# Performance work log

Hardware: AMD Instinct MI355X
Metric: run time of the kernel (lower is better)

## Reference

```python
import jax, jax.numpy as jnp
from jax import lax
import numpy as np

B, T, F, U, O = 512, 512, 128, 256, 32  # batch, max_t, joint feature dim, lstm units, n_output


def setup_inputs() -> dict:
    key = jax.random.key(0)
    k = jax.random.split(key, 6)
    return {
        "x_joint": jax.random.normal(k[0], (B, T, F), dtype=jnp.float32),
        "Wx": jax.random.normal(k[1], (F, 4 * U), dtype=jnp.float32) / np.sqrt(F).astype(np.float32),
        "Wh": jax.random.normal(k[2], (U, 4 * U), dtype=jnp.float32) / np.sqrt(U).astype(np.float32),
        "b": jnp.zeros((4 * U,), dtype=jnp.float32),
        "Wo": jax.random.normal(k[3], (U, O), dtype=jnp.float32) / np.sqrt(U).astype(np.float32),
        "bo": jnp.zeros((O,), dtype=jnp.float32),
        "seq_lengths": jax.random.randint(k[4], (B,), 0, T, dtype=jnp.int32),
    }


def reference(x_joint, Wx, Wh, b, Wo, bo, seq_lengths):
    """Masked LSTM decoder scan with per-step Dense projection.

    Flax nn.RNN(DecoderLSTMCell): LSTMCell gates i,f,g,o then Dense(n_output).
    With return_carry=True + seq_lengths, flax only uses seq_lengths to slice the
    final carry, which RNNSurrogate discards; outputs are the full per-step
    predictions, so seq_lengths does not enter the returned math.
    """
    bsz, t, _ = x_joint.shape
    units = Wh.shape[0]
    # precompute input contribution to all 4 gates: [B, T, 4U]
    x_proj = jnp.einsum('btf,fg->btg', x_joint, Wx) + b
    c0 = jnp.zeros((bsz, units), dtype=x_joint.dtype)
    h0 = jnp.zeros((bsz, units), dtype=x_joint.dtype)

    def step(carry, xt):
        c, h = carry
        z = xt + h @ Wh  # [B, 4U]
        i, f, g, o = jnp.split(z, 4, axis=-1)
        c = jax.nn.sigmoid(f) * c + jax.nn.sigmoid(i) * jnp.tanh(g)
        h = jax.nn.sigmoid(o) * jnp.tanh(c)
        y = h @ Wo + bo  # per-step Dense projection
        return (c, h), y

    _, ys = lax.scan(step, (c0, h0), x_proj.transpose(1, 0, 2))  # ys: [T, B, O]
    return ys.transpose(1, 0, 2)  # [B, T, O]
```

## Files before the change

### kernel.cpp

```cpp
#include <hip/hip_runtime.h>
#include <stdint.h>

#define BB 512
#define TT 512
#define FF 128
#define UU 256

typedef float f32x4 __attribute__((ext_vector_type(4)));
typedef short short8 __attribute__((ext_vector_type(8)));
typedef int int4v __attribute__((ext_vector_type(4)));
typedef float float4v __attribute__((ext_vector_type(4)));
typedef unsigned short ushort4v __attribute__((ext_vector_type(4)));

__device__ __forceinline__ unsigned short f2bf(float f) {
  union { float f; uint32_t u; } v; v.f = f;
  uint32_t u = v.u;
  u += 0x7fffu + ((u >> 16) & 1u);
  return (unsigned short)(u >> 16);
}
__device__ __forceinline__ float fast_rcp(float x) { return __builtin_amdgcn_rcpf(x); }
__device__ __forceinline__ float sigmoidf_(float x) { return fast_rcp(1.f + __expf(-x)); }
__device__ __forceinline__ float tanhf_(float x) { return 1.f - 2.f * fast_rcp(1.f + __expf(2.f * x)); }

__global__ void prep_w(const float* __restrict__ Wx, const float* __restrict__ Wh,
                       const float* __restrict__ Wo,
                       unsigned short* __restrict__ Wt, unsigned short* __restrict__ Wot,
                       int* __restrict__ xch) {
  int bidx = blockIdx.x;
  int tid = threadIdx.x;
  if (bidx < 1024) {
    int n = bidx, k = tid;
    float v = (k < FF) ? Wx[(size_t)k * 1024 + n] : Wh[(size_t)(k - FF) * 1024 + n];
    Wt[(size_t)n * 384 + k] = f2bf(v);
  } else if (bidx == 1024) {
    for (int i = tid; i < 32 * 256; i += 384) {
      int o = i >> 8, u = i & 255;
      Wot[o * 256 + u] = f2bf(Wo[(size_t)u * 32 + o]);
    }
  } else {
    int base = (bidx - 1025) * 2048;
    for (int i = tid; i < 2048; i += 384) xch[base + i] = 0;
  }
}

__global__ void conv_x(const float* __restrict__ xf, unsigned short* __restrict__ xb) {
  size_t i = (size_t)blockIdx.x * 1024 + (size_t)threadIdx.x * 4;
  float4v v = *(const float4v*)(xf + i);
  ushort4v o;
  o.x = f2bf(v.x); o.y = f2bf(v.y); o.z = f2bf(v.z); o.w = f2bf(v.w);
  *(ushort4v*)(xb + i) = o;
}

__device__ __forceinline__ short8 load_xfrag(const unsigned short* p) {
  return *(const short8*)p;
}
__device__ __forceinline__ short8 load_xfrag(const float* p) {
  float4v lo = *(const float4v*)p;
  float4v hi = *(const float4v*)(p + 4);
  union { short8 v; unsigned short s[8]; } a;
  a.s[0] = f2bf(lo.x); a.s[1] = f2bf(lo.y); a.s[2] = f2bf(lo.z); a.s[3] = f2bf(lo.w);
  a.s[4] = f2bf(hi.x); a.s[5] = f2bf(hi.y); a.s[6] = f2bf(hi.z); a.s[7] = f2bf(hi.w);
  return a.v;
}

__device__ __forceinline__ void store_sc01(int* p, int v) {
  asm volatile("global_store_dword %0, %1, off sc0 sc1" :: "v"(p), "v"(v) : "memory");
}
__device__ __forceinline__ uint32_t pk2(int lo, int hi) {
  return ((uint32_t)lo >> 16) | ((uint32_t)hi & 0xffff0000u);
}

template <int HALF, typename XT>
__device__ __forceinline__ void lstm_core(const XT* __restrict__ x,
                                          const unsigned short* __restrict__ Wt,
                                          const float* __restrict__ bvec,
                                          unsigned short* __restrict__ h_hist,
                                          int* __restrict__ xch, int bid, char* lds) {
  const int mt = bid & 31;
  const int tid = threadIdx.x;
  const int w = tid >> 6, l = tid & 63;
  const int lr = l & 15, lhi = l >> 4;
  const int b0 = mt * 16;
  const int uloc = HALF * 128 + w * 16 + lr;
  char* hlds = lds + 131072;
  char* plds = lds + 139264;

#pragma unroll
  for (int g = 0; g < 4; ++g)
#pragma unroll
    for (int kk = 0; kk < 4; ++kk) {
      const unsigned short* wp = Wt + (size_t)(g * 256 + uloc) * 384 + kk * 32 + 8 * lhi;
      *(short8*)(lds + ((size_t)((w * 16 + g * 4 + kk) * 64 + l)) * 16) = *(const short8*)wp;
    }

  short8 Bh[4][8];
#pragma unroll
  for (int g = 0; g < 4; ++g) {
    const unsigned short* wp = Wt + (size_t)(g * 256 + uloc) * 384 + FF + 8 * lhi;
#pragma unroll
    for (int kf = 0; kf < 8; ++kf) Bh[g][kf] = *(const short8*)(wp + kf * 32);
  }
  float bias[4];
#pragma unroll
  for (int g = 0; g < 4; ++g) bias[g] = bvec[g * 256 + uloc];
  float cst[4] = {0.f, 0.f, 0.f, 0.f};

  constexpr int kf_own = HALF * 4;
  constexpr int kf_par = (1 - HALF) * 4;

  const int rtile = (mt * 2 + (1 - HALF)) * 2;
  const int wtile = (mt * 2 + HALF) * 2;

  const int prow = tid >> 5;
  const int pwbyte = (prow * 256 + (tid & 31) * 8) ^ ((prow & 7) << 4);

  short8 xa[4];
  {
    const XT* xp = x + ((size_t)(b0 + lr) * TT + 0) * FF + 8 * lhi;
#pragma unroll
    for (int kk = 0; kk < 4; ++kk) xa[kk] = load_xfrag(xp + kk * 32);
  }
  __syncthreads();

#pragma unroll 1
  for (int t = 0; t < TT; ++t) {
    const int cur = t & 1, nxt = cur ^ 1;

    f32x4 acc[4];
#pragma unroll
    for (int g = 0; g < 4; ++g) { f32x4 a4 = {bias[g], bias[g], bias[g], bias[g]}; acc[g] = a4; }

    if (t > 0) {
      short8 ho[4];
#pragma unroll
      for (int ko = 0; ko < 4; ++ko) {
        const int byte = cur * 4096 + lr * 256 + ((ko * 64 + lhi * 16) ^ ((lr & 7) << 4));
        ho[ko] = *(const short8*)(hlds + byte);
      }
#pragma unroll
      for (int ko = 0; ko < 4; ++ko)
#pragma unroll
        for (int g = 0; g < 4; ++g)
          acc[g] = __builtin_amdgcn_mfma_f32_16x16x32_bf16(ho[ko], Bh[g][kf_own + ko], acc[g], 0, 0, 0);
    }

#pragma unroll
    for (int kk = 0; kk < 4; ++kk) {
      short8 bx[4];
#pragma unroll
      for (int g = 0; g < 4; ++g)
        bx[g] = *(const short8*)(lds + ((size_t)((w * 16 + g * 4 + kk) * 64 + l)) * 16);
#pragma unroll
      for (int g = 0; g < 4; ++g)
        acc[g] = __builtin_amdgcn_mfma_f32_16x16x32_bf16(xa[kk], bx[g], acc[g], 0, 0, 0);
    }

    {
      const int tn = (t + 1 < TT) ? t + 1 : t;
      const XT* xp = x + ((size_t)(b0 + lr) * TT + tn) * FF + 8 * lhi;
#pragma unroll
      for (int kk = 0; kk < 4; ++kk) xa[kk] = load_xfrag(xp + kk * 32);
    }

    if (t > 0) {
      const int* pp = xch + (rtile + cur) * 2048 + 4 * tid;
      int4v a;
      for (;;) {
        asm volatile("global_load_dwordx4 %0, %1, off sc0 sc1\n\ts_waitcnt vmcnt(0)"
                     : "=&v"(a) : "v"(pp) : "memory");
        int m = ((a.x ^ t) | (a.y ^ t) | (a.z ^ t) | (a.w ^ t)) & 0xffff;
        if (__all(m == 0)) break;
      }
      __builtin_amdgcn_sched_barrier(0);

      uint32_t d0 = pk2(a.x, a.y), d1 = pk2(a.z, a.w);
      *(uint64_t*)(plds + pwbyte) = ((uint64_t)d1 << 32) | d0;
      __syncthreads();

      short8 hq[4];
#pragma unroll
      for (int ko = 0; ko < 4; ++ko) {
        const int byte = (lr * 256 + lhi * 16 + ko * 64) ^ ((lr & 7) << 4);
        hq[ko] = *(const short8*)(plds + byte);
      }
#pragma unroll
      for (int ko = 0; ko < 4; ++ko)
#pragma unroll
        for (int g = 0; g < 4; ++g)
          acc[g] = __builtin_amdgcn_mfma_f32_16x16x32_bf16(hq[ko], Bh[g][kf_par + ko], acc[g], 0, 0, 0);
    }

    unsigned short hs[4];
#pragma unroll
    for (int r = 0; r < 4; ++r) {
      float zi = acc[0][r], zf = acc[1][r], zg = acc[2][r], zo = acc[3][r];
      float si = sigmoidf_(zi), sf = sigmoidf_(zf), so = sigmoidf_(zo);
      float tg = tanhf_(zg);
      float cn = sf * cst[r] + si * tg;
      cst[r] = cn;
      hs[r] = f2bf(so * tanhf_(cn));
    }

    const int wb = (wtile + nxt) * 2048 + w * 16 + lr;
    unsigned short* hw = h_hist + (size_t)(t + 1) * (BB * UU) + uloc;
#pragma unroll
    for (int r = 0; r < 4; ++r) {
      const int row = 4 * lhi + r;
      const int byte = nxt * 4096 + row * 256 + (((w * 16 + lr) * 2) ^ ((row & 7) << 4));
      *(unsigned short*)(hlds + byte) = hs[r];
      store_sc01(xch + wb + row * 128, ((int)(uint32_t)hs[r] << 16) | (t + 1));
      hw[(size_t)(b0 + row) * UU] = hs[r];
    }

    __syncthreads();
  }
}

template <typename XT>
__global__ void __launch_bounds__(512, 2)
lstm_main10(const XT* __restrict__ x, const unsigned short* __restrict__ Wt,
            const float* __restrict__ bvec, unsigned short* __restrict__ h_hist,
            int* __restrict__ xch) {
  __shared__ __align__(16) char lds[143360];
  const int bid = blockIdx.x;
  if (bid < 32) lstm_core<0, XT>(x, Wt, bvec, h_hist, xch, bid, lds);
  else          lstm_core<1, XT>(x, Wt, bvec, h_hist, xch, bid, lds);
}

__global__ void __launch_bounds__(256)
y_gemm(const unsigned short* __restrict__ h_hist, const unsigned short* __restrict__ Wot,
       const float* __restrict__ bo, float* __restrict__ out) {
  int gw = (int)((blockIdx.x * 256 + threadIdx.x) >> 6);
  int l = threadIdx.x & 63;
  int lr = l & 15, lhi = l >> 4;
  int b = gw >> 5;
  int t0 = (gw & 31) * 16;

  short8 Wf[2][8];
#pragma unroll
  for (int n = 0; n < 2; ++n) {
    const unsigned short* wp = Wot + (n * 16 + lr) * 256 + 8 * lhi;
#pragma unroll
    for (int kk = 0; kk < 8; ++kk) Wf[n][kk] = *(const short8*)(wp + kk * 32);
  }
  f32x4 acc[2];
#pragma unroll
  for (int n = 0; n < 2; ++n) {
    float bb = bo[n * 16 + lr];
    f32x4 a4 = {bb, bb, bb, bb};
    acc[n] = a4;
  }
  const unsigned short* hp =
      h_hist + ((size_t)(t0 + lr + 1) * BB + b) * UU + 8 * lhi;
#pragma unroll
  for (int kk = 0; kk < 8; ++kk) {
    short8 a = *(const short8*)(hp + kk * 32);
#pragma unroll
    for (int n = 0; n < 2; ++n)
      acc[n] = __builtin_amdgcn_mfma_f32_16x16x32_bf16(a, Wf[n][kk], acc[n], 0, 0, 0);
  }
#pragma unroll
  for (int n = 0; n < 2; ++n) {
    int o = n * 16 + lr;
#pragma unroll
    for (int r = 0; r < 4; ++r) {
      int t = t0 + 4 * lhi + r;
      out[((size_t)b * TT + t) * 32 + o] = acc[n][r];
    }
  }
}

extern "C" void kernel_launch(void* const* d_in, const int* in_sizes, int n_in,
                              void* d_out, int out_size, void* d_ws, size_t ws_size,
                              hipStream_t stream) {
  const float* x  = (const float*)d_in[0];
  const float* Wx = (const float*)d_in[1];
  const float* Wh = (const float*)d_in[2];
  const float* bv = (const float*)d_in[3];
  const float* Wo = (const float*)d_in[4];
  const float* bo = (const float*)d_in[5];

  char* ws = (char*)d_ws;
  size_t off = 0;
  int* xch = (int*)(ws + off);                          off += (size_t)262144 * 4;
  unsigned short* h_hist = (unsigned short*)(ws + off); off += (size_t)513 * BB * UU * 2;
  unsigned short* Wt384  = (unsigned short*)(ws + off); off += (size_t)1024 * 384 * 2;
  unsigned short* Wot    = (unsigned short*)(ws + off); off += (size_t)32 * 256 * 2;
  off = (off + 255) & ~(size_t)255;
  unsigned short* xb = (unsigned short*)(ws + off);
  const size_t need_xb = off + (size_t)BB * TT * FF * 2;

  prep_w<<<1153, 384, 0, stream>>>(Wx, Wh, Wo, Wt384, Wot, xch);
  if (ws_size >= need_xb) {
    conv_x<<<32768, 256, 0, stream>>>(x, xb);
    lstm_main10<unsigned short><<<64, 512, 0, stream>>>(xb, Wt384, bv, h_hist, xch);
  } else {
    lstm_main10<float><<<64, 512, 0, stream>>>(x, Wt384, bv, h_hist, xch);
  }
  y_gemm<<<4096, 256, 0, stream>>>(h_hist, Wot, bo, (float*)d_out);
}
```

Measured before the change: 1.483 ms.

## Fuse output projection into LSTM recurrence and drop h history buffer

Computes the per-step Dense projection inside the recurrent kernel: wave 0 of each block reuses the previous step's h fragments, already in registers, with Wo staged in LDS, and writes outputs lagged by two steps, with an epilogue for the last two timesteps. This removes the large global h_hist write (513×B×U bf16) and the separate y_gemm launch. It also issues the exchange load early, before the MFMA work, to overlap its latency, and reorders the xch stores ahead of the LDS writes. The cost is extra MFMA and LDS work on wave 0 on the serial critical path, plus more LDS per block.

```diff
diff --git a/kernel.cpp b/kernel.cpp
--- a/kernel.cpp
+++ b/kernel.cpp
@@ -73,8 +73,10 @@
 template <int HALF, typename XT>
 __device__ __forceinline__ void lstm_core(const XT* __restrict__ x,
                                           const unsigned short* __restrict__ Wt,
+                                          const unsigned short* __restrict__ Wot,
                                           const float* __restrict__ bvec,
-                                          unsigned short* __restrict__ h_hist,
+                                          const float* __restrict__ bo,
+                                          float* __restrict__ out,
                                           int* __restrict__ xch, int bid, char* lds) {
   const int mt = bid & 31;
   const int tid = threadIdx.x;
@@ -84,6 +86,7 @@
   const int uloc = HALF * 128 + w * 16 + lr;
   char* hlds = lds + 131072;
   char* plds = lds + 139264;
+  char* wolds = lds + 143360;
 
 #pragma unroll
   for (int g = 0; g < 4; ++g)
@@ -92,6 +95,13 @@
       const unsigned short* wp = Wt + (size_t)(g * 256 + uloc) * 384 + kk * 32 + 8 * lhi;
       *(short8*)(lds + ((size_t)((w * 16 + g * 4 + kk) * 64 + l)) * 16) = *(const short8*)wp;
     }
+  if (w == 0) {
+#pragma unroll
+    for (int kf = 0; kf < 8; ++kf) {
+      const unsigned short* src = Wot + (size_t)(HALF * 16 + lr) * 256 + kf * 32 + 8 * lhi;
+      *(short8*)(wolds + (size_t)(kf * 64 + l) * 16) = *(const short8*)src;
+    }
+  }
 
   short8 Bh[4][8];
 #pragma unroll
@@ -103,6 +113,7 @@
   float bias[4];
 #pragma unroll
   for (int g = 0; g < 4; ++g) bias[g] = bvec[g * 256 + uloc];
+  const float bob = bo[HALF * 16 + lr];
   float cst[4] = {0.f, 0.f, 0.f, 0.f};
 
   constexpr int kf_own = HALF * 4;
@@ -113,6 +124,8 @@
 
   const int prow = tid >> 5;
   const int pwbyte = (prow * 256 + (tid & 31) * 8) ^ ((prow & 7) << 4);
+
+  short8 ho[4], hq[4];
 
   short8 xa[4];
   {
@@ -125,13 +138,36 @@
 #pragma unroll 1
   for (int t = 0; t < TT; ++t) {
     const int cur = t & 1, nxt = cur ^ 1;
+    const int* pp = xch + (rtile + cur) * 2048 + 4 * tid;
+
+    int4v a;
+    if (t > 0) {
+      asm volatile("global_load_dwordx4 %0, %1, off sc0 sc1"
+                   : "=&v"(a) : "v"(pp) : "memory");
+    }
+
+    if (t >= 2 && w == 0) {
+      f32x4 yacc = {bob, bob, bob, bob};
+#pragma unroll
+      for (int ko = 0; ko < 4; ++ko) {
+        short8 wf = *(const short8*)(wolds + (size_t)((kf_own + ko) * 64 + l) * 16);
+        yacc = __builtin_amdgcn_mfma_f32_16x16x32_bf16(ho[ko], wf, yacc, 0, 0, 0);
+      }
+#pragma unroll
+      for (int ko = 0; ko < 4; ++ko) {
+        short8 wf = *(const short8*)(wolds + (size_t)((kf_par + ko) * 64 + l) * 16);
+        yacc = __builtin_amdgcn_mfma_f32_16x16x32_bf16(hq[ko], wf, yacc, 0, 0, 0);
+      }
+#pragma unroll
+      for (int r = 0; r < 4; ++r)
+        out[((size_t)(b0 + 4 * lhi + r) * TT + (t - 2)) * 32 + HALF * 16 + lr] = yacc[r];
+    }
 
     f32x4 acc[4];
 #pragma unroll
     for (int g = 0; g < 4; ++g) { f32x4 a4 = {bias[g], bias[g], bias[g], bias[g]}; acc[g] = a4; }
 
     if (t > 0) {
-      short8 ho[4];
 #pragma unroll
       for (int ko = 0; ko < 4; ++ko) {
         const int byte = cur * 4096 + lr * 256 + ((ko * 64 + lhi * 16) ^ ((lr & 7) << 4));
@@ -163,21 +199,17 @@
     }
 
     if (t > 0) {
-      const int* pp = xch + (rtile + cur) * 2048 + 4 * tid;
-      int4v a;
-      for (;;) {
+      asm volatile("s_waitcnt vmcnt(0)" ::: "memory");
+      __builtin_amdgcn_sched_barrier(0);
+      while (!__all(((((a.x ^ t) | (a.y ^ t)) | ((a.z ^ t) | (a.w ^ t))) & 0xffff) == 0)) {
         asm volatile("global_load_dwordx4 %0, %1, off sc0 sc1\n\ts_waitcnt vmcnt(0)"
                      : "=&v"(a) : "v"(pp) : "memory");
-        int m = ((a.x ^ t) | (a.y ^ t) | (a.z ^ t) | (a.w ^ t)) & 0xffff;
-        if (__all(m == 0)) break;
       }
       __builtin_amdgcn_sched_barrier(0);
 
       uint32_t d0 = pk2(a.x, a.y), d1 = pk2(a.z, a.w);
       *(uint64_t*)(plds + pwbyte) = ((uint64_t)d1 << 32) | d0;
       __syncthreads();
-
-      short8 hq[4];
 #pragma unroll
       for (int ko = 0; ko < 4; ++ko) {
         const int byte = (lr * 256 + lhi * 16 + ko * 64) ^ ((lr & 7) << 4);
@@ -202,72 +234,78 @@
     }
 
     const int wb = (wtile + nxt) * 2048 + w * 16 + lr;
-    unsigned short* hw = h_hist + (size_t)(t + 1) * (BB * UU) + uloc;
+#pragma unroll
+    for (int r = 0; r < 4; ++r)
+      store_sc01(xch + wb + (4 * lhi + r) * 128, ((int)(uint32_t)hs[r] << 16) | (t + 1));
 #pragma unroll
     for (int r = 0; r < 4; ++r) {
       const int row = 4 * lhi + r;
       const int byte = nxt * 4096 + row * 256 + (((w * 16 + lr) * 2) ^ ((row & 7) << 4));
       *(unsigned short*)(hlds + byte) = hs[r];
-      store_sc01(xch + wb + row * 128, ((int)(uint32_t)hs[r] << 16) | (t + 1));
-      hw[(size_t)(b0 + row) * UU] = hs[r];
     }
 
     __syncthreads();
+  }
+
+  if (w == 0) {
+    f32x4 yacc = {bob, bob, bob, bob};
+#pragma unroll
+    for (int ko = 0; ko < 4; ++ko) {
+      short8 wf = *(const short8*)(wolds + (size_t)((kf_own + ko) * 64 + l) * 16);
+      yacc = __builtin_amdgcn_mfma_f32_16x16x32_bf16(ho[ko], wf, yacc, 0, 0, 0);
+    }
+#pragma unroll
+    for (int ko = 0; ko < 4; ++ko) {
+      short8 wf = *(const short8*)(wolds + (size_t)((kf_par + ko) * 64 + l) * 16);
+      yacc = __builtin_amdgcn_mfma_f32_16x16x32_bf16(hq[ko], wf, yacc, 0, 0, 0);
+    }
+#pragma unroll
+    for (int r = 0; r < 4; ++r)
+      out[((size_t)(b0 + 4 * lhi + r) * TT + (TT - 2)) * 32 + HALF * 16 + lr] = yacc[r];
+  }
+  {
+    const int* pp = xch + (rtile + 0) * 2048 + 4 * tid;
+    int4v a;
+    do {
+      asm volatile("global_load_dwordx4 %0, %1, off sc0 sc1\n\ts_waitcnt vmcnt(0)"
+                   : "=&v"(a) : "v"(pp) : "memory");
+    } while (!__all(((((a.x ^ TT) | (a.y ^ TT)) | ((a.z ^ TT) | (a.w ^ TT))) & 0xffff) == 0));
+    __builtin_amdgcn_sched_barrier(0);
+    uint32_t d0 = pk2(a.x, a.y), d1 = pk2(a.z, a.w);
+    *(uint64_t*)(plds + pwbyte) = ((uint64_t)d1 << 32) | d0;
+    __syncthreads();
+    if (w == 0) {
+      f32x4 yacc = {bob, bob, bob, bob};
+#pragma unroll
+      for (int ko = 0; ko < 4; ++ko) {
+        const int byte = 0 * 4096 + lr * 256 + ((ko * 64 + lhi * 16) ^ ((lr & 7) << 4));
+        short8 hof = *(const short8*)(hlds + byte);
+        short8 wf = *(const short8*)(wolds + (size_t)((kf_own + ko) * 64 + l) * 16);
+        yacc = __builtin_amdgcn_mfma_f32_16x16x32_bf16(hof, wf, yacc, 0, 0, 0);
+      }
+#pragma unroll
+      for (int ko = 0; ko < 4; ++ko) {
+        const int byte = (lr * 256 + lhi * 16 + ko * 64) ^ ((lr & 7) << 4);
+        short8 hqf = *(const short8*)(plds + byte);
+        short8 wf = *(const short8*)(wolds + (size_t)((kf_par + ko) * 64 + l) * 16);
+        yacc = __builtin_amdgcn_mfma_f32_16x16x32_bf16(hqf, wf, yacc, 0, 0, 0);
+      }
+#pragma unroll
+      for (int r = 0; r < 4; ++r)
+        out[((size_t)(b0 + 4 * lhi + r) * TT + (TT - 1)) * 32 + HALF * 16 + lr] = yacc[r];
+    }
   }
 }
 
 template <typename XT>
 __global__ void __launch_bounds__(512, 2)
-lstm_main10(const XT* __restrict__ x, const unsigned short* __restrict__ Wt,
-            const float* __restrict__ bvec, unsigned short* __restrict__ h_hist,
-            int* __restrict__ xch) {
-  __shared__ __align__(16) char lds[143360];
+lstm_main14(const XT* __restrict__ x, const unsigned short* __restrict__ Wt,
+            const unsigned short* __restrict__ Wot, const float* __restrict__ bvec,
+            const float* __restrict__ bo, float* __restrict__ out, int* __restrict__ xch) {
+  __shared__ __align__(16) char lds[151552];
   const int bid = blockIdx.x;
-  if (bid < 32) lstm_core<0, XT>(x, Wt, bvec, h_hist, xch, bid, lds);
-  else          lstm_core<1, XT>(x, Wt, bvec, h_hist, xch, bid, lds);
-}
-
-__global__ void __launch_bounds__(256)
-y_gemm(const unsigned short* __restrict__ h_hist, const unsigned short* __restrict__ Wot,
-       const float* __restrict__ bo, float* __restrict__ out) {
-  int gw = (int)((blockIdx.x * 256 + threadIdx.x) >> 6);
-  int l = threadIdx.x & 63;
-  int lr = l & 15, lhi = l >> 4;
-  int b = gw >> 5;
-  int t0 = (gw & 31) * 16;
-
-  short8 Wf[2][8];
-#pragma unroll
-  for (int n = 0; n < 2; ++n) {
-    const unsigned short* wp = Wot + (n * 16 + lr) * 256 + 8 * lhi;
-#pragma unroll
-    for (int kk = 0; kk < 8; ++kk) Wf[n][kk] = *(const short8*)(wp + kk * 32);
-  }
-  f32x4 acc[2];
-#pragma unroll
-  for (int n = 0; n < 2; ++n) {
-    float bb = bo[n * 16 + lr];
-    f32x4 a4 = {bb, bb, bb, bb};
-    acc[n] = a4;
-  }
-  const unsigned short* hp =
-      h_hist + ((size_t)(t0 + lr + 1) * BB + b) * UU + 8 * lhi;
-#pragma unroll
-  for (int kk = 0; kk < 8; ++kk) {
-    short8 a = *(const short8*)(hp + kk * 32);
-#pragma unroll
-    for (int n = 0; n < 2; ++n)
-      acc[n] = __builtin_amdgcn_mfma_f32_16x16x32_bf16(a, Wf[n][kk], acc[n], 0, 0, 0);
-  }
-#pragma unroll
-  for (int n = 0; n < 2; ++n) {
-    int o = n * 16 + lr;
-#pragma unroll
-    for (int r = 0; r < 4; ++r) {
-      int t = t0 + 4 * lhi + r;
-      out[((size_t)b * TT + t) * 32 + o] = acc[n][r];
-    }
-  }
+  if (bid < 32) lstm_core<0, XT>(x, Wt, Wot, bvec, bo, out, xch, bid, lds);
+  else          lstm_core<1, XT>(x, Wt, Wot, bvec, bo, out, xch, bid, lds);
 }
 
 extern "C" void kernel_launch(void* const* d_in, const int* in_sizes, int n_in,
@@ -283,9 +321,8 @@
   char* ws = (char*)d_ws;
   size_t off = 0;
   int* xch = (int*)(ws + off);                          off += (size_t)262144 * 4;
-  unsigned short* h_hist = (unsigned short*)(ws + off); off += (size_t)513 * BB * UU * 2;
-  unsigned short* Wt384  = (unsigned short*)(ws + off); off += (size_t)1024 * 384 * 2;
-  unsigned short* Wot    = (unsigned short*)(ws + off); off += (size_t)32 * 256 * 2;
+  unsigned short* Wt384 = (unsigned short*)(ws + off);  off += (size_t)1024 * 384 * 2;
+  unsigned short* Wot   = (unsigned short*)(ws + off);  off += (size_t)32 * 256 * 2;
   off = (off + 255) & ~(size_t)255;
   unsigned short* xb = (unsigned short*)(ws + off);
   const size_t need_xb = off + (size_t)BB * TT * FF * 2;
@@ -293,9 +330,8 @@
   prep_w<<<1153, 384, 0, stream>>>(Wx, Wh, Wo, Wt384, Wot, xch);
   if (ws_size >= need_xb) {
     conv_x<<<32768, 256, 0, stream>>>(x, xb);
-    lstm_main10<unsigned short><<<64, 512, 0, stream>>>(xb, Wt384, bv, h_hist, xch);
+    lstm_main14<unsigned short><<<64, 512, 0, stream>>>(xb, Wt384, Wot, bv, bo, (float*)d_out, xch);
   } else {
-    lstm_main10<float><<<64, 512, 0, stream>>>(x, Wt384, bv, h_hist, xch);
-  }
-  y_gemm<<<4096, 256, 0, stream>>>(h_hist, Wot, bo, (float*)d_out);
-}
+    lstm_main14<float><<<64, 512, 0, stream>>>(x, Wt384, Wot, bv, bo, (float*)d_out, xch);
+  }
+}
```

New measurement: 1.678 ms. 13.2% more time.
